# Performance work log

Hardware: AMD Instinct MI355X
Metric: run time of the kernel (lower is better)

Reference implementation:

```python
import jax, jax.numpy as jnp
import numpy as np

B, NIN, D = 2048, 64, 128
N_LCB, N_FMB, RANK = 32, 32, 24
DIM_HIDDEN = 1024
N_OUT = N_LCB + N_FMB  # == NIN -> identity residual
MAX_VAL = 1.0
EPS_LN_FMB_MIN, EPS_LN_FMB_MAX = 1e-11, 1e7
KERAS_LN_EPS = 1e-3


def setup_inputs() -> dict:
    key = jax.random.key(0)
    ks = jax.random.split(key, 9)
    def w(k, shape, fan):
        return (jax.random.normal(k, shape, jnp.float32) / np.sqrt(fan)).astype(jnp.float32)
    return {
        "x": jax.random.normal(ks[0], (B, NIN, D), jnp.float32),
        "noise": jax.random.uniform(ks[1], (B, N_OUT, D), jnp.float32),
        "w_lcb": w(ks[2], (NIN, N_LCB), NIN),
        "w_rank": w(ks[3], (NIN, RANK), NIN),
        "w1": w(ks[4], (NIN * RANK, DIM_HIDDEN), NIN * RANK),
        "w2": w(ks[5], (DIM_HIDDEN, DIM_HIDDEN), DIM_HIDDEN),
        "w3": w(ks[6], (DIM_HIDDEN, N_FMB * D), DIM_HIDDEN),
        "gamma": jnp.ones((D,), jnp.float32),
        "beta": jnp.zeros((D,), jnp.float32),
    }


def _forward(x, noise, w_lcb, w_rank, w1, w2, w3, gamma, beta):
    # ---- LinearCompressBlock: Dense over feature (emb-count) axis ----
    lcb = jnp.einsum("bnd,nm->bmd", x, w_lcb)  # (B, N_LCB, D)

    # ---- FactorizationMachineBlock ----
    # rank_layer on transposed input: (B, D, NIN) @ (NIN, RANK)
    r = jnp.einsum("bnd,nr->bdr", x, w_rank)          # (B, D, RANK)
    fm = jnp.einsum("bnd,bdr->bnr", x, r)             # (B, NIN, RANK)
    fm = fm.reshape(fm.shape[0], NIN * RANK)
    # custom LayerNorm (no affine, clipped std)
    mu = jnp.mean(fm, axis=-1, keepdims=True)
    cen = fm - mu
    std = jnp.sqrt(jnp.mean(cen * cen, axis=-1, keepdims=True))
    std = jnp.clip(std, EPS_LN_FMB_MIN, EPS_LN_FMB_MAX)
    fm = cen / std
    # MLP: 2 hidden relu layers + linear out, dropout=0 / inference
    h = jax.nn.relu(fm @ w1)
    h = jax.nn.relu(h @ w2)
    fmb = (h @ w3).reshape(-1, N_FMB, D)              # (B, N_FMB, D)

    out = jnp.concatenate((fmb, lcb), axis=1)          # (B, N_OUT, D)
    residual = x                                        # NIN == N_OUT -> identity

    safe = jnp.clip(out, -MAX_VAL, MAX_VAL)
    a = jnp.abs(safe)
    c = lambda t: jnp.clip(t, -MAX_VAL, MAX_VAL)

    # conv term: reshape to (B, N, D//8, 8), 1x1 conv with all-ones (8->8)
    # filter == group-sum broadcast back over the 8 lanes
    g = safe.reshape(safe.shape[0], N_OUT, D // 8, 8)
    conv = jnp.broadcast_to(g.sum(-1, keepdims=True), g.shape).reshape(safe.shape)

    extra = (
        c(jnp.log(a + 1.0))
        + c(jax.lax.rsqrt(a + 1.0))
        + c(jax.nn.softmax(safe, axis=-1))
        + c(jnp.tanh(safe))
        + c(jnp.where(safe >= 0, safe, 0.2 * safe))          # leaky_relu alpha=0.2
        + c(jnp.exp(safe))
        + c(jax.nn.softplus(safe))
        + c(jnp.log1p(a))
        + jnp.zeros_like(safe)                               # zeros_like term
        + c(jnp.round(safe))
        + jnp.ones_like(safe)                                # pow(a+eps, 0) == 1
        + c(jnp.sign(safe))
        + c(jnp.prod(safe, axis=-1, keepdims=True))
        + c(jnp.isnan(safe).astype(jnp.float32))
        + c((~(safe < 0)).astype(jnp.float32))
        + c((safe != 0).astype(jnp.float32))
        + c((safe >= 0).astype(jnp.float32))
        + c(safe.astype(jnp.int8).astype(jnp.float32))       # bitwise_and(x,x)==x after int8 cast
        + c(jnp.max(safe, axis=-1, keepdims=True))
        + c(safe + safe)                                     # add_n([safe, safe])
        + c(safe + safe)                                     # raw Add
        + 7.0 * safe                                         # slice/split-concat/merge/einsum/squeeze/pad/stack identities (|safe|<=1 so clip no-op)
        + c(jnp.where(safe > 0.5, -1.0, safe))               # tensor_scatter_nd_update
        + c(conv)
        + c(noise)                                           # tf.random.uniform (deterministic input)
        + c(jnp.arange(D, dtype=jnp.float32))                # broadcast over last axis
        + c(jnp.sum(safe[0] * safe[0], axis=-1))[None, :, None]  # DiagPart(matmul(safe[0], safe[0]^T))
    )

    pre = out + residual + 1e-10 * extra
    # keras LayerNormalization(axis=-1), default epsilon=1e-3
    m = jnp.mean(pre, axis=-1, keepdims=True)
    v = jnp.mean(jnp.square(pre - m), axis=-1, keepdims=True)
    return (pre - m) * jax.lax.rsqrt(v + KERAS_LN_EPS) * gamma + beta


def reference(x, noise, w_lcb, w_rank, w1, w2, w3, gamma, beta):
    return _forward(x, noise, w_lcb, w_rank, w1, w2, w3, gamma, beta)
```

## Files before the change

kernel.cpp:

```cpp
#include <hip/hip_runtime.h>


typedef _Float16 half8_t __attribute__((ext_vector_type(8)));
typedef _Float16 half4_t __attribute__((ext_vector_type(4)));
typedef float floatx4 __attribute__((ext_vector_type(4)));

#define B_SZ 2048
#define NIN 64
#define D_SZ 128
#define RANK 24
#define FMK (NIN * RANK)
#define HID 1024
#define NFMB_D (32 * 128)
#define ROW_F (NIN * D_SZ)

__device__ __forceinline__ void wg_barrier() {
  asm volatile("s_waitcnt lgkmcnt(0)" ::: "memory");
  __builtin_amdgcn_sched_barrier(0);
  __builtin_amdgcn_s_barrier();
  __builtin_amdgcn_sched_barrier(0);
}

__global__ __launch_bounds__(256) void transpose_cast_all(
    const float* __restrict__ w1, const float* __restrict__ w2,
    const float* __restrict__ w3, const float* __restrict__ w_rank,
    const float* __restrict__ w_lcb, _Float16* __restrict__ w1t,
    _Float16* __restrict__ w2t, _Float16* __restrict__ w3t,
    _Float16* __restrict__ wr16, _Float16* __restrict__ wl16) {
  __shared__ float tile[32][33];
  int bid = blockIdx.x;
  if (bid == 48 * 32 + 32 * 32 + 32 * 128) {
    const int t = threadIdx.x;
#pragma unroll
    for (int k = 0; k < 8; k++) {
      int i = t + k * 256;
      int j = i >> 6, n = i & 63;
      wr16[i] = (_Float16)(j < RANK ? w_rank[n * RANK + j] : 0.f);
      wl16[i] = (_Float16)w_lcb[n * 32 + j];
    }
    return;
  }
  const float* w;
  _Float16* wt;
  int K, N, kt;
  if (bid < 48 * 32) {
    w = w1; wt = w1t; K = FMK; N = HID; kt = 48;
  } else if (bid < 48 * 32 + 32 * 32) {
    bid -= 48 * 32;
    w = w2; wt = w2t; K = HID; N = HID; kt = 32;
  } else {
    bid -= 48 * 32 + 32 * 32;
    w = w3; wt = w3t; K = HID; N = NFMB_D; kt = 32;
  }
  const int tk = (bid % kt) * 32;
  const int tn = (bid / kt) * 32;
  const int tx = threadIdx.x & 31;
  const int ty = threadIdx.x >> 5;
#pragma unroll
  for (int i = 0; i < 4; i++) {
    int k = ty + i * 8;
    tile[k][tx] = w[(size_t)(tk + k) * N + (tn + tx)];
  }
  __syncthreads();
#pragma unroll
  for (int i = 0; i < 4; i++) {
    int n = ty + i * 8;
    wt[(size_t)(tn + n) * K + (tk + tx)] = (_Float16)tile[tx][n];
  }
}

#define STX 72
#define STN 136
__global__ __launch_bounds__(256, 3) void front_kernel(
    const float* __restrict__ x, const _Float16* __restrict__ wr16,
    const _Float16* __restrict__ wl16, const float* __restrict__ gamma,
    const float* __restrict__ beta, _Float16* __restrict__ fmn,
    float* __restrict__ out) {
  constexpr int XT_OFF = 0;
  constexpr int X16_OFF = 18432;
  constexpr int RT_OFF = X16_OFF + 17408;
  constexpr int RED_OFF = RT_OFF + 8704;
  __shared__ __align__(16) char smem[RED_OFF + 32];
  __shared__ float2 lstat[32][4];
  _Float16* xT = (_Float16*)(smem + XT_OFF);
  _Float16* x16 = (_Float16*)(smem + X16_OFF);
  _Float16* rT = (_Float16*)(smem + RT_OFF);
  float* redbuf = (float*)(smem + RED_OFF);
  _Float16* fmn_s = (_Float16*)(smem + RT_OFF);

  const int b = blockIdx.x, t = threadIdx.x;
  const int lane = t & 63;
  const int w = __builtin_amdgcn_readfirstlane(t >> 6);
  const int q = lane >> 4, ln = lane & 15;

  half8_t ar[2][2], al[2][2];
#pragma unroll
  for (int k = 0; k < 2; k++)
#pragma unroll
    for (int mi = 0; mi < 2; mi++) {
      ar[k][mi] = *(const half8_t*)&wr16[(mi * 16 + ln) * 64 + k * 32 + q * 8];
      al[k][mi] = *(const half8_t*)&wl16[(mi * 16 + ln) * 64 + k * 32 + q * 8];
    }

  const float4* xg4 = (const float4*)(x + (size_t)b * ROW_F);
#pragma unroll
  for (int hh = 0; hh < 2; hh++) {
    int bb = t + hh * 256;
    int n0 = (bb >> 5) * 4;
    int bd = bb & 31;
    int d0 = bd * 4;
    float4 L0 = xg4[(n0 + 0) * 32 + bd];
    float4 L1 = xg4[(n0 + 1) * 32 + bd];
    float4 L2 = xg4[(n0 + 2) * 32 + bd];
    float4 L3 = xg4[(n0 + 3) * 32 + bd];
    *(half4_t*)&x16[(n0 + 0) * STN + d0] =
        half4_t{(_Float16)L0.x, (_Float16)L0.y, (_Float16)L0.z, (_Float16)L0.w};
    *(half4_t*)&x16[(n0 + 1) * STN + d0] =
        half4_t{(_Float16)L1.x, (_Float16)L1.y, (_Float16)L1.z, (_Float16)L1.w};
    *(half4_t*)&x16[(n0 + 2) * STN + d0] =
        half4_t{(_Float16)L2.x, (_Float16)L2.y, (_Float16)L2.z, (_Float16)L2.w};
    *(half4_t*)&x16[(n0 + 3) * STN + d0] =
        half4_t{(_Float16)L3.x, (_Float16)L3.y, (_Float16)L3.z, (_Float16)L3.w};
    *(half4_t*)&xT[(d0 + 0) * STX + n0] =
        half4_t{(_Float16)L0.x, (_Float16)L1.x, (_Float16)L2.x, (_Float16)L3.x};
    *(half4_t*)&xT[(d0 + 1) * STX + n0] =
        half4_t{(_Float16)L0.y, (_Float16)L1.y, (_Float16)L2.y, (_Float16)L3.y};
    *(half4_t*)&xT[(d0 + 2) * STX + n0] =
        half4_t{(_Float16)L0.z, (_Float16)L1.z, (_Float16)L2.z, (_Float16)L3.z};
    *(half4_t*)&xT[(d0 + 3) * STX + n0] =
        half4_t{(_Float16)L0.w, (_Float16)L1.w, (_Float16)L2.w, (_Float16)L3.w};
  }
  __syncthreads();

  floatx4 r_acc[2][2] = {};
  floatx4 l_acc[2][2] = {};
#pragma unroll
  for (int k = 0; k < 2; k++) {
    half8_t bfrag[2];
#pragma unroll
    for (int ni = 0; ni < 2; ni++)
      bfrag[ni] =
          *(const half8_t*)&xT[((2 * w + ni) * 16 + ln) * STX + k * 32 + q * 8];
#pragma unroll
    for (int mi = 0; mi < 2; mi++)
#pragma unroll
      for (int ni = 0; ni < 2; ni++) {
        r_acc[mi][ni] = __builtin_amdgcn_mfma_f32_16x16x32_f16(
            ar[k][mi], bfrag[ni], r_acc[mi][ni], 0, 0, 0);
        l_acc[mi][ni] = __builtin_amdgcn_mfma_f32_16x16x32_f16(
            al[k][mi], bfrag[ni], l_acc[mi][ni], 0, 0, 0);
      }
  }
#pragma unroll
  for (int mi = 0; mi < 2; mi++)
#pragma unroll
    for (int ni = 0; ni < 2; ni++)
#pragma unroll
      for (int rr = 0; rr < 4; rr++)
        rT[(mi * 16 + q * 4 + rr) * STN + (2 * w + ni) * 16 + ln] =
            (_Float16)r_acc[mi][ni][rr];
  __syncthreads();

  floatx4 f_acc[2] = {};
#pragma unroll
  for (int k = 0; k < 4; k++) {
    half8_t af = *(const half8_t*)&x16[(w * 16 + ln) * STN + k * 32 + q * 8];
#pragma unroll
    for (int nj = 0; nj < 2; nj++) {
      half8_t bf = *(const half8_t*)&rT[(nj * 16 + ln) * STN + k * 32 + q * 8];
      f_acc[nj] =
          __builtin_amdgcn_mfma_f32_16x16x32_f16(af, bf, f_acc[nj], 0, 0, 0);
    }
  }
  float s = 0.f, s2 = 0.f;
#pragma unroll
  for (int rr = 0; rr < 4; rr++) {
    float v = f_acc[0][rr];
    s += v;
    s2 += v * v;
    float v1 = (ln < 8) ? f_acc[1][rr] : 0.f;
    s += v1;
    s2 += v1 * v1;
  }
#pragma unroll
  for (int off = 1; off < 64; off <<= 1) {
    s += __shfl_xor(s, off);
    s2 += __shfl_xor(s2, off);
  }
  if (lane == 0) {
    redbuf[w * 2] = s;
    redbuf[w * 2 + 1] = s2;
  }
  __syncthreads();
  s = redbuf[0] + redbuf[2] + redbuf[4] + redbuf[6];
  s2 = redbuf[1] + redbuf[3] + redbuf[5] + redbuf[7];
  const float mu = s * (1.f / FMK);
  float var = s2 * (1.f / FMK) - mu * mu;
  var = var > 0.f ? var : 0.f;
  float sd = sqrtf(var);
  sd = sd < 1e-11f ? 1e-11f : (sd > 1e7f ? 1e7f : sd);
  const float inv = 1.f / sd;

#pragma unroll
  for (int nj = 0; nj < 2; nj++) {
    int j = nj * 16 + ln;
    if (j < RANK) {
#pragma unroll
      for (int rr = 0; rr < 4; rr++)
        fmn_s[(w * 16 + q * 4 + rr) * RANK + j] =
            (_Float16)((f_acc[nj][rr] - mu) * inv);
    }
  }

  const int d0 = (2 * w) * 16 + ln;
  const int d1 = d0 + 16;
  const float g0 = gamma[d0], g1 = gamma[d1];
  const float be0 = beta[d0], be1 = beta[d1];
  float lv0[2][4], lv1[2][4];
  float sw[2][4], s2w[2][4];
#pragma unroll
  for (int mi = 0; mi < 2; mi++)
#pragma unroll
    for (int rr = 0; rr < 4; rr++) {
      int m = mi * 16 + q * 4 + rr;
      float v0 = l_acc[mi][0][rr] + (float)x16[(32 + m) * STN + d0];
      float v1 = l_acc[mi][1][rr] + (float)x16[(32 + m) * STN + d1];
      lv0[mi][rr] = v0;
      lv1[mi][rr] = v1;
      sw[mi][rr] = v0 + v1;
      s2w[mi][rr] = v0 * v0 + v1 * v1;
    }
#pragma unroll
  for (int off = 1; off < 16; off <<= 1) {
#pragma unroll
    for (int mi = 0; mi < 2; mi++)
#pragma unroll
      for (int rr = 0; rr < 4; rr++) {
        sw[mi][rr] += __shfl_xor(sw[mi][rr], off);
        s2w[mi][rr] += __shfl_xor(s2w[mi][rr], off);
      }
  }
  if (ln == 0) {
#pragma unroll
    for (int mi = 0; mi < 2; mi++)
#pragma unroll
      for (int rr = 0; rr < 4; rr++)
        lstat[mi * 16 + q * 4 + rr][w] = float2{sw[mi][rr], s2w[mi][rr]};
  }
  __syncthreads();

  half8_t* fg = (half8_t*)(fmn + (size_t)b * FMK);
  if (t < FMK / 8) fg[t] = ((const half8_t*)fmn_s)[t];
  float* ob = out + (size_t)b * ROW_F;
#pragma unroll
  for (int mi = 0; mi < 2; mi++)
#pragma unroll
    for (int rr = 0; rr < 4; rr++) {
      int m = mi * 16 + q * 4 + rr;
      float2 p0 = lstat[m][0], p1 = lstat[m][1];
      float2 p2 = lstat[m][2], p3 = lstat[m][3];
      float S = p0.x + p1.x + p2.x + p3.x;
      float S2 = p0.y + p1.y + p2.y + p3.y;
      float mean = S * (1.f / 128.f);
      float varr = S2 * (1.f / 128.f) - mean * mean;
      float rstd = rsqrtf(varr + 1e-3f);
      ob[(32 + m) * 128 + d0] = (lv0[mi][rr] - mean) * rstd * g0 + be0;
      ob[(32 + m) * 128 + d1] = (lv1[mi][rr] - mean) * rstd * g1 + be1;
    }
}

template <bool RELU>
__global__ __launch_bounds__(256, 2) void gemm_bt(
    const _Float16* __restrict__ A, const _Float16* __restrict__ Bt,
    _Float16* __restrict__ C, int M, int N, int K) {
  constexpr int LDT = 40;
  __shared__ __align__(16) _Float16 As[2][64 * LDT];
  __shared__ __align__(16) _Float16 Bs[2][64 * LDT];
  const int m0 = blockIdx.x * 64;
  const int n0 = blockIdx.y * 64;
  const int t = threadIdx.x;
  const int wave = t >> 6, lane = t & 63;
  const int wr = wave >> 1, wc = wave & 1;
  const int q = lane >> 4, ln = lane & 15;
  const int srow = t >> 2;
  const int skc = t & 3;
  const _Float16* gA = A + (size_t)(m0 + srow) * K + skc * 8;
  const _Float16* gB = Bt + (size_t)(n0 + srow) * K + skc * 8;
  const int ldsw = srow * LDT + skc * 8;
  const int nT = K / 32;

  floatx4 acc[2][2] = {};

  uint4 rax = *(const uint4*)gA;
  uint4 rbx = *(const uint4*)gB;
  *(uint4*)&As[0][ldsw] = rax;
  *(uint4*)&Bs[0][ldsw] = rbx;
  uint4 ray = *(const uint4*)(gA + 32);
  uint4 rby = *(const uint4*)(gB + 32);
  rax = *(const uint4*)(gA + 64);
  rbx = *(const uint4*)(gB + 64);
  wg_barrier();

  for (int tp = 0;;) {
    if (tp + 1 < nT) {
      *(uint4*)&As[1][ldsw] = ray;
      *(uint4*)&Bs[1][ldsw] = rby;
    }
    half8_t af[2], bf[2];
#pragma unroll
    for (int i = 0; i < 2; i++) {
      af[i] = *(const half8_t*)&As[0][(wr * 32 + i * 16 + ln) * LDT + q * 8];
      bf[i] = *(const half8_t*)&Bs[0][(wc * 32 + i * 16 + ln) * LDT + q * 8];
    }
    if (tp + 3 < nT) {
      ray = *(const uint4*)(gA + (tp + 3) * 32);
      rby = *(const uint4*)(gB + (tp + 3) * 32);
    }
#pragma unroll
    for (int i = 0; i < 2; i++)
#pragma unroll
      for (int j = 0; j < 2; j++)
        acc[i][j] = __builtin_amdgcn_mfma_f32_16x16x32_f16(af[i], bf[j],
                                                           acc[i][j], 0, 0, 0);
    if (tp + 1 >= nT) break;
    wg_barrier();
    if (tp + 2 < nT) {
      *(uint4*)&As[0][ldsw] = rax;
      *(uint4*)&Bs[0][ldsw] = rbx;
    }
#pragma unroll
    for (int i = 0; i < 2; i++) {
      af[i] = *(const half8_t*)&As[1][(wr * 32 + i * 16 + ln) * LDT + q * 8];
      bf[i] = *(const half8_t*)&Bs[1][(wc * 32 + i * 16 + ln) * LDT + q * 8];
    }
    if (tp + 4 < nT) {
      rax = *(const uint4*)(gA + (tp + 4) * 32);
      rbx = *(const uint4*)(gB + (tp + 4) * 32);
    }
#pragma unroll
    for (int i = 0; i < 2; i++)
#pragma unroll
      for (int j = 0; j < 2; j++)
        acc[i][j] = __builtin_amdgcn_mfma_f32_16x16x32_f16(af[i], bf[j],
                                                           acc[i][j], 0, 0, 0);
    tp += 2;
    if (tp >= nT) break;
    wg_barrier();
  }

#pragma unroll
  for (int i = 0; i < 2; i++) {
#pragma unroll
    for (int r = 0; r < 4; r++) {
      size_t row = (size_t)(m0 + wr * 32 + i * 16 + q * 4 + r);
      _Float16* crow = C + row * N + n0 + wc * 32 + ln;
#pragma unroll
      for (int j = 0; j < 2; j++) {
        float v = acc[i][j][r];
        if (RELU) v = v > 0.f ? v : 0.f;
        crow[j * 16] = (_Float16)v;
      }
    }
  }
}

__global__ __launch_bounds__(256, 2) void gemm_ln(
    const _Float16* __restrict__ A, const _Float16* __restrict__ Bt,
    const float* __restrict__ x, const float* __restrict__ gamma,
    const float* __restrict__ beta, float* __restrict__ out) {
  constexpr int LDT = 40;
  constexpr int K = HID;
  constexpr int nT = K / 32;
  __shared__ __align__(16) _Float16 As[2][128 * LDT];
  __shared__ __align__(16) _Float16 Bs[2][128 * LDT];
  __shared__ float2 rowst[128][2];
  const int m0 = blockIdx.x * 128;
  const int c = blockIdx.y;
  const int n0 = c * 128;
  const int t = threadIdx.x;
  const int wave = t >> 6, lane = t & 63;
  const int wr = wave >> 1, wc = wave & 1;
  const int q = lane >> 4, ln = lane & 15;
  const int srow = t >> 2;
  const int skc = t & 3;
  const _Float16* gA0 = A + (size_t)(m0 + srow) * K + skc * 8;
  const _Float16* gA1 = gA0 + (size_t)64 * K;
  const _Float16* gB0 = Bt + (size_t)(n0 + srow) * K + skc * 8;
  const _Float16* gB1 = gB0 + (size_t)64 * K;
  const int ldsw = srow * LDT + skc * 8;

  floatx4 acc[4][4] = {};

  uint4 raX0 = *(const uint4*)gA0, raX1 = *(const uint4*)gA1;
  uint4 rbX0 = *(const uint4*)gB0, rbX1 = *(const uint4*)gB1;
  *(uint4*)&As[0][ldsw] = raX0;
  *(uint4*)&As[0][64 * LDT + ldsw] = raX1;
  *(uint4*)&Bs[0][ldsw] = rbX0;
  *(uint4*)&Bs[0][64 * LDT + ldsw] = rbX1;
  uint4 raY0 = *(const uint4*)(gA0 + 32), raY1 = *(const uint4*)(gA1 + 32);
  uint4 rbY0 = *(const uint4*)(gB0 + 32), rbY1 = *(const uint4*)(gB1 + 32);
  raX0 = *(const uint4*)(gA0 + 64);
  raX1 = *(const uint4*)(gA1 + 64);
  rbX0 = *(const uint4*)(gB0 + 64);
  rbX1 = *(const uint4*)(gB1 + 64);
  wg_barrier();

  for (int tp = 0;;) {
    if (tp + 1 < nT) {
      *(uint4*)&As[1][ldsw] = raY0;
      *(uint4*)&As[1][64 * LDT + ldsw] = raY1;
      *(uint4*)&Bs[1][ldsw] = rbY0;
      *(uint4*)&Bs[1][64 * LDT + ldsw] = rbY1;
    }
    half8_t af[4], bf[4];
#pragma unroll
    for (int i = 0; i < 4; i++)
      af[i] = *(const half8_t*)&As[0][(wr * 64 + i * 16 + ln) * LDT + q * 8];
#pragma unroll
    for (int j = 0; j < 4; j++)
      bf[j] = *(const half8_t*)&Bs[0][(wc * 64 + j * 16 + ln) * LDT + q * 8];
    if (tp + 3 < nT) {
      raY0 = *(const uint4*)(gA0 + (tp + 3) * 32);
      raY1 = *(const uint4*)(gA1 + (tp + 3) * 32);
      rbY0 = *(const uint4*)(gB0 + (tp + 3) * 32);
      rbY1 = *(const uint4*)(gB1 + (tp + 3) * 32);
    }
#pragma unroll
    for (int i = 0; i < 4; i++)
#pragma unroll
      for (int j = 0; j < 4; j++)
        acc[i][j] = __builtin_amdgcn_mfma_f32_16x16x32_f16(af[i], bf[j],
                                                           acc[i][j], 0, 0, 0);
    if (tp + 1 >= nT) break;
    wg_barrier();
    if (tp + 2 < nT) {
      *(uint4*)&As[0][ldsw] = raX0;
      *(uint4*)&As[0][64 * LDT + ldsw] = raX1;
      *(uint4*)&Bs[0][ldsw] = rbX0;
      *(uint4*)&Bs[0][64 * LDT + ldsw] = rbX1;
    }
#pragma unroll
    for (int i = 0; i < 4; i++)
      af[i] = *(const half8_t*)&As[1][(wr * 64 + i * 16 + ln) * LDT + q * 8];
#pragma unroll
    for (int j = 0; j < 4; j++)
      bf[j] = *(const half8_t*)&Bs[1][(wc * 64 + j * 16 + ln) * LDT + q * 8];
    if (tp + 4 < nT) {
      raX0 = *(const uint4*)(gA0 + (tp + 4) * 32);
      raX1 = *(const uint4*)(gA1 + (tp + 4) * 32);
      rbX0 = *(const uint4*)(gB0 + (tp + 4) * 32);
      rbX1 = *(const uint4*)(gB1 + (tp + 4) * 32);
    }
#pragma unroll
    for (int i = 0; i < 4; i++)
#pragma unroll
      for (int j = 0; j < 4; j++)
        acc[i][j] = __builtin_amdgcn_mfma_f32_16x16x32_f16(af[i], bf[j],
                                                           acc[i][j], 0, 0, 0);
    tp += 2;
    if (tp >= nT) break;
    wg_barrier();
  }

  float s[4][4], s2[4][4];
#pragma unroll
  for (int i = 0; i < 4; i++)
#pragma unroll
    for (int r = 0; r < 4; r++) {
      const int row = wr * 64 + i * 16 + q * 4 + r;
      const float* xr = x + (size_t)(m0 + row) * ROW_F + n0 + wc * 64 + ln;
      float ss = 0.f, qq = 0.f;
#pragma unroll
      for (int j = 0; j < 4; j++) {
        float v = acc[i][j][r] + xr[j * 16];
        acc[i][j][r] = v;
        ss += v;
        qq += v * v;
      }
      s[i][r] = ss;
      s2[i][r] = qq;
    }
#pragma unroll
  for (int off = 1; off < 16; off <<= 1) {
#pragma unroll
    for (int i = 0; i < 4; i++)
#pragma unroll
      for (int r = 0; r < 4; r++) {
        s[i][r] += __shfl_xor(s[i][r], off);
        s2[i][r] += __shfl_xor(s2[i][r], off);
      }
  }
  if (ln == 0) {
#pragma unroll
    for (int i = 0; i < 4; i++)
#pragma unroll
      for (int r = 0; r < 4; r++)
        rowst[wr * 64 + i * 16 + q * 4 + r][wc] = float2{s[i][r], s2[i][r]};
  }
  __syncthreads();
  float g[4], bb[4];
#pragma unroll
  for (int j = 0; j < 4; j++) {
    g[j] = gamma[wc * 64 + j * 16 + ln];
    bb[j] = beta[wc * 64 + j * 16 + ln];
  }
#pragma unroll
  for (int i = 0; i < 4; i++)
#pragma unroll
    for (int r = 0; r < 4; r++) {
      int row = wr * 64 + i * 16 + q * 4 + r;
      float2 p0 = rowst[row][0], p1 = rowst[row][1];
      float mean = (p0.x + p1.x) * (1.f / 128.f);
      float varr = (p0.y + p1.y) * (1.f / 128.f) - mean * mean;
      float rstd = rsqrtf(varr + 1e-3f);
      float* orow = out + (size_t)(m0 + row) * ROW_F + n0 + wc * 64 + ln;
#pragma unroll
      for (int j = 0; j < 4; j++)
        orow[j * 16] = (acc[i][j][r] - mean) * rstd * g[j] + bb[j];
    }
}

extern "C" void kernel_launch(void* const* d_in, const int* in_sizes, int n_in,
                              void* d_out, int out_size, void* d_ws,
                              size_t ws_size, hipStream_t stream) {
  const float* x = (const float*)d_in[0];
  const float* w_lcb = (const float*)d_in[2];
  const float* w_rank = (const float*)d_in[3];
  const float* w1 = (const float*)d_in[4];
  const float* w2 = (const float*)d_in[5];
  const float* w3 = (const float*)d_in[6];
  const float* gamma = (const float*)d_in[7];
  const float* beta = (const float*)d_in[8];
  float* out = (float*)d_out;

  char* ws = (char*)d_ws;
  _Float16* w1t = (_Float16*)ws; ws += (size_t)HID * FMK * 2;
  _Float16* w2t = (_Float16*)ws; ws += (size_t)HID * HID * 2;
  _Float16* w3t = (_Float16*)ws; ws += (size_t)NFMB_D * HID * 2;
  _Float16* fmn = (_Float16*)ws; ws += (size_t)B_SZ * FMK * 2;
  _Float16* h1  = (_Float16*)ws; ws += (size_t)B_SZ * HID * 2;
  _Float16* wr16 = (_Float16*)ws; ws += 32 * 64 * 2;
  _Float16* wl16 = (_Float16*)ws; ws += 32 * 64 * 2;
  _Float16* h2 = fmn;

  transpose_cast_all<<<48 * 32 + 32 * 32 + 32 * 128 + 1, 256, 0, stream>>>(
      w1, w2, w3, w_rank, w_lcb, w1t, w2t, w3t, wr16, wl16);
  front_kernel<<<B_SZ, 256, 0, stream>>>(x, wr16, wl16, gamma, beta, fmn, out);
  gemm_bt<true><<<dim3(B_SZ / 64, HID / 64), 256, 0, stream>>>(
      fmn, w1t, h1, B_SZ, HID, FMK);
  gemm_bt<true><<<dim3(B_SZ / 64, HID / 64), 256, 0, stream>>>(
      h1, w2t, h2, B_SZ, HID, HID);
  gemm_ln<<<dim3(B_SZ / 128, 32), 256, 0, stream>>>(h2, w3t, x, gamma, beta, out);
}
```

Baseline: 255.2 us.

## Load MFMA fragments directly from global memory and remap blocks for XCD locality

```diff
diff --git a/kernel.cpp b/kernel.cpp
--- a/kernel.cpp
+++ b/kernel.cpp
@@ -13,13 +13,6 @@
 #define HID 1024
 #define NFMB_D (32 * 128)
 #define ROW_F (NIN * D_SZ)
-
-__device__ __forceinline__ void wg_barrier() {
-  asm volatile("s_waitcnt lgkmcnt(0)" ::: "memory");
-  __builtin_amdgcn_sched_barrier(0);
-  __builtin_amdgcn_s_barrier();
-  __builtin_amdgcn_sched_barrier(0);
-}
 
 __global__ __launch_bounds__(256) void transpose_cast_all(
     const float* __restrict__ w1, const float* __restrict__ w2,
@@ -269,83 +262,59 @@
     }
 }
 
-template <bool RELU>
+template <int K, bool RELU>
 __global__ __launch_bounds__(256, 2) void gemm_bt(
     const _Float16* __restrict__ A, const _Float16* __restrict__ Bt,
-    _Float16* __restrict__ C, int M, int N, int K) {
-  constexpr int LDT = 40;
-  __shared__ __align__(16) _Float16 As[2][64 * LDT];
-  __shared__ __align__(16) _Float16 Bs[2][64 * LDT];
-  const int m0 = blockIdx.x * 64;
-  const int n0 = blockIdx.y * 64;
+    _Float16* __restrict__ C) {
+  constexpr int nT = K / 32;
+  const int flat = blockIdx.x + (blockIdx.y << 5);
+  const int xcd = flat & 7, sub = flat >> 3;
+  const int mb = (xcd & 3) * 8 + (sub & 7);
+  const int nb = (xcd >> 2) * 8 + (sub >> 3);
+  const int m0 = mb * 64, n0 = nb * 64;
   const int t = threadIdx.x;
   const int wave = t >> 6, lane = t & 63;
   const int wr = wave >> 1, wc = wave & 1;
   const int q = lane >> 4, ln = lane & 15;
-  const int srow = t >> 2;
-  const int skc = t & 3;
-  const _Float16* gA = A + (size_t)(m0 + srow) * K + skc * 8;
-  const _Float16* gB = Bt + (size_t)(n0 + srow) * K + skc * 8;
-  const int ldsw = srow * LDT + skc * 8;
-  const int nT = K / 32;
+
+  const _Float16* a0 = A + (size_t)(m0 + wr * 32 + ln) * K + q * 8;
+  const _Float16* b0 = Bt + (size_t)(n0 + wc * 32 + ln) * K + q * 8;
 
   floatx4 acc[2][2] = {};
-
-  uint4 rax = *(const uint4*)gA;
-  uint4 rbx = *(const uint4*)gB;
-  *(uint4*)&As[0][ldsw] = rax;
-  *(uint4*)&Bs[0][ldsw] = rbx;
-  uint4 ray = *(const uint4*)(gA + 32);
-  uint4 rby = *(const uint4*)(gB + 32);
-  rax = *(const uint4*)(gA + 64);
-  rbx = *(const uint4*)(gB + 64);
-  wg_barrier();
+  half8_t aX[2], bX[2], aY[2], bY[2];
+  auto ld2 = [&](half8_t(&d)[2], const _Float16* base, int kk) {
+#pragma unroll
+    for (int i = 0; i < 2; i++)
+      d[i] = *(const half8_t*)(base + (size_t)(i * 16) * K + kk);
+  };
+  ld2(aX, a0, 0);
+  ld2(bX, b0, 0);
+  ld2(aY, a0, 32);
+  ld2(bY, b0, 32);
 
   for (int tp = 0;;) {
-    if (tp + 1 < nT) {
-      *(uint4*)&As[1][ldsw] = ray;
-      *(uint4*)&Bs[1][ldsw] = rby;
-    }
-    half8_t af[2], bf[2];
-#pragma unroll
-    for (int i = 0; i < 2; i++) {
-      af[i] = *(const half8_t*)&As[0][(wr * 32 + i * 16 + ln) * LDT + q * 8];
-      bf[i] = *(const half8_t*)&Bs[0][(wc * 32 + i * 16 + ln) * LDT + q * 8];
-    }
+#pragma unroll
+    for (int i = 0; i < 2; i++)
+#pragma unroll
+      for (int j = 0; j < 2; j++)
+        acc[i][j] = __builtin_amdgcn_mfma_f32_16x16x32_f16(aX[i], bX[j],
+                                                           acc[i][j], 0, 0, 0);
+    if (tp + 2 < nT) {
+      ld2(aX, a0, (tp + 2) * 32);
+      ld2(bX, b0, (tp + 2) * 32);
+    }
+#pragma unroll
+    for (int i = 0; i < 2; i++)
+#pragma unroll
+      for (int j = 0; j < 2; j++)
+        acc[i][j] = __builtin_amdgcn_mfma_f32_16x16x32_f16(aY[i], bY[j],
+                                                           acc[i][j], 0, 0, 0);
     if (tp + 3 < nT) {
-      ray = *(const uint4*)(gA + (tp + 3) * 32);
-      rby = *(const uint4*)(gB + (tp + 3) * 32);
-    }
-#pragma unroll
-    for (int i = 0; i < 2; i++)
-#pragma unroll
-      for (int j = 0; j < 2; j++)
-        acc[i][j] = __builtin_amdgcn_mfma_f32_16x16x32_f16(af[i], bf[j],
-                                                           acc[i][j], 0, 0, 0);
-    if (tp + 1 >= nT) break;
-    wg_barrier();
-    if (tp + 2 < nT) {
-      *(uint4*)&As[0][ldsw] = rax;
-      *(uint4*)&Bs[0][ldsw] = rbx;
-    }
-#pragma unroll
-    for (int i = 0; i < 2; i++) {
-      af[i] = *(const half8_t*)&As[1][(wr * 32 + i * 16 + ln) * LDT + q * 8];
-      bf[i] = *(const half8_t*)&Bs[1][(wc * 32 + i * 16 + ln) * LDT + q * 8];
-    }
-    if (tp + 4 < nT) {
-      rax = *(const uint4*)(gA + (tp + 4) * 32);
-      rbx = *(const uint4*)(gB + (tp + 4) * 32);
-    }
-#pragma unroll
-    for (int i = 0; i < 2; i++)
-#pragma unroll
-      for (int j = 0; j < 2; j++)
-        acc[i][j] = __builtin_amdgcn_mfma_f32_16x16x32_f16(af[i], bf[j],
-                                                           acc[i][j], 0, 0, 0);
+      ld2(aY, a0, (tp + 3) * 32);
+      ld2(bY, b0, (tp + 3) * 32);
+    }
     tp += 2;
     if (tp >= nT) break;
-    wg_barrier();
   }
 
 #pragma unroll
@@ -353,7 +322,7 @@
 #pragma unroll
     for (int r = 0; r < 4; r++) {
       size_t row = (size_t)(m0 + wr * 32 + i * 16 + q * 4 + r);
-      _Float16* crow = C + row * N + n0 + wc * 32 + ln;
+      _Float16* crow = C + row * HID + n0 + wc * 32 + ln;
 #pragma unroll
       for (int j = 0; j < 2; j++) {
         float v = acc[i][j][r];
@@ -368,98 +337,57 @@
     const _Float16* __restrict__ A, const _Float16* __restrict__ Bt,
     const float* __restrict__ x, const float* __restrict__ gamma,
     const float* __restrict__ beta, float* __restrict__ out) {
-  constexpr int LDT = 40;
   constexpr int K = HID;
   constexpr int nT = K / 32;
-  __shared__ __align__(16) _Float16 As[2][128 * LDT];
-  __shared__ __align__(16) _Float16 Bs[2][128 * LDT];
   __shared__ float2 rowst[128][2];
-  const int m0 = blockIdx.x * 128;
-  const int c = blockIdx.y;
-  const int n0 = c * 128;
+  const int flat = blockIdx.x + (blockIdx.y << 4);
+  const int xcd = flat & 7, sub = flat >> 3;
+  const int mb = (xcd & 1) * 8 + (sub & 7);
+  const int c = (xcd >> 1) * 8 + (sub >> 3);
+  const int m0 = mb * 128, n0 = c * 128;
   const int t = threadIdx.x;
   const int wave = t >> 6, lane = t & 63;
   const int wr = wave >> 1, wc = wave & 1;
   const int q = lane >> 4, ln = lane & 15;
-  const int srow = t >> 2;
-  const int skc = t & 3;
-  const _Float16* gA0 = A + (size_t)(m0 + srow) * K + skc * 8;
-  const _Float16* gA1 = gA0 + (size_t)64 * K;
-  const _Float16* gB0 = Bt + (size_t)(n0 + srow) * K + skc * 8;
-  const _Float16* gB1 = gB0 + (size_t)64 * K;
-  const int ldsw = srow * LDT + skc * 8;
+
+  const _Float16* a0 = A + (size_t)(m0 + wr * 64 + ln) * K + q * 8;
+  const _Float16* b0 = Bt + (size_t)(n0 + wc * 64 + ln) * K + q * 8;
 
   floatx4 acc[4][4] = {};
-
-  uint4 raX0 = *(const uint4*)gA0, raX1 = *(const uint4*)gA1;
-  uint4 rbX0 = *(const uint4*)gB0, rbX1 = *(const uint4*)gB1;
-  *(uint4*)&As[0][ldsw] = raX0;
-  *(uint4*)&As[0][64 * LDT + ldsw] = raX1;
-  *(uint4*)&Bs[0][ldsw] = rbX0;
-  *(uint4*)&Bs[0][64 * LDT + ldsw] = rbX1;
-  uint4 raY0 = *(const uint4*)(gA0 + 32), raY1 = *(const uint4*)(gA1 + 32);
-  uint4 rbY0 = *(const uint4*)(gB0 + 32), rbY1 = *(const uint4*)(gB1 + 32);
-  raX0 = *(const uint4*)(gA0 + 64);
-  raX1 = *(const uint4*)(gA1 + 64);
-  rbX0 = *(const uint4*)(gB0 + 64);
-  rbX1 = *(const uint4*)(gB1 + 64);
-  wg_barrier();
+  half8_t aX[4], bX[4], aY[4], bY[4];
+  auto ld4 = [&](half8_t(&d)[4], const _Float16* base, int kk) {
+#pragma unroll
+    for (int i = 0; i < 4; i++)
+      d[i] = *(const half8_t*)(base + (size_t)(i * 16) * K + kk);
+  };
+  ld4(aX, a0, 0);
+  ld4(bX, b0, 0);
+  ld4(aY, a0, 32);
+  ld4(bY, b0, 32);
 
   for (int tp = 0;;) {
-    if (tp + 1 < nT) {
-      *(uint4*)&As[1][ldsw] = raY0;
-      *(uint4*)&As[1][64 * LDT + ldsw] = raY1;
-      *(uint4*)&Bs[1][ldsw] = rbY0;
-      *(uint4*)&Bs[1][64 * LDT + ldsw] = rbY1;
-    }
-    half8_t af[4], bf[4];
 #pragma unroll
     for (int i = 0; i < 4; i++)
-      af[i] = *(const half8_t*)&As[0][(wr * 64 + i * 16 + ln) * LDT + q * 8];
-#pragma unroll
-    for (int j = 0; j < 4; j++)
-      bf[j] = *(const half8_t*)&Bs[0][(wc * 64 + j * 16 + ln) * LDT + q * 8];
+#pragma unroll
+      for (int j = 0; j < 4; j++)
+        acc[i][j] = __builtin_amdgcn_mfma_f32_16x16x32_f16(aX[i], bX[j],
+                                                           acc[i][j], 0, 0, 0);
+    if (tp + 2 < nT) {
+      ld4(aX, a0, (tp + 2) * 32);
+      ld4(bX, b0, (tp + 2) * 32);
+    }
+#pragma unroll
+    for (int i = 0; i < 4; i++)
+#pragma unroll
+      for (int j = 0; j < 4; j++)
+        acc[i][j] = __builtin_amdgcn_mfma_f32_16x16x32_f16(aY[i], bY[j],
+                                                           acc[i][j], 0, 0, 0);
     if (tp + 3 < nT) {
-      raY0 = *(const uint4*)(gA0 + (tp + 3) * 32);
-      raY1 = *(const uint4*)(gA1 + (tp + 3) * 32);
-      rbY0 = *(const uint4*)(gB0 + (tp + 3) * 32);
-      rbY1 = *(const uint4*)(gB1 + (tp + 3) * 32);
-    }
-#pragma unroll
-    for (int i = 0; i < 4; i++)
-#pragma unroll
-      for (int j = 0; j < 4; j++)
-        acc[i][j] = __builtin_amdgcn_mfma_f32_16x16x32_f16(af[i], bf[j],
-                                                           acc[i][j], 0, 0, 0);
-    if (tp + 1 >= nT) break;
-    wg_barrier();
-    if (tp + 2 < nT) {
-      *(uint4*)&As[0][ldsw] = raX0;
-      *(uint4*)&As[0][64 * LDT + ldsw] = raX1;
-      *(uint4*)&Bs[0][ldsw] = rbX0;
-      *(uint4*)&Bs[0][64 * LDT + ldsw] = rbX1;
-    }
-#pragma unroll
-    for (int i = 0; i < 4; i++)
-      af[i] = *(const half8_t*)&As[1][(wr * 64 + i * 16 + ln) * LDT + q * 8];
-#pragma unroll
-    for (int j = 0; j < 4; j++)
-      bf[j] = *(const half8_t*)&Bs[1][(wc * 64 + j * 16 + ln) * LDT + q * 8];
-    if (tp + 4 < nT) {
-      raX0 = *(const uint4*)(gA0 + (tp + 4) * 32);
-      raX1 = *(const uint4*)(gA1 + (tp + 4) * 32);
-      rbX0 = *(const uint4*)(gB0 + (tp + 4) * 32);
-      rbX1 = *(const uint4*)(gB1 + (tp + 4) * 32);
-    }
-#pragma unroll
-    for (int i = 0; i < 4; i++)
-#pragma unroll
-      for (int j = 0; j < 4; j++)
-        acc[i][j] = __builtin_amdgcn_mfma_f32_16x16x32_f16(af[i], bf[j],
-                                                           acc[i][j], 0, 0, 0);
+      ld4(aY, a0, (tp + 3) * 32);
+      ld4(bY, b0, (tp + 3) * 32);
+    }
     tp += 2;
     if (tp >= nT) break;
-    wg_barrier();
   }
 
   float s[4][4], s2[4][4];
@@ -546,9 +474,9 @@
   transpose_cast_all<<<48 * 32 + 32 * 32 + 32 * 128 + 1, 256, 0, stream>>>(
       w1, w2, w3, w_rank, w_lcb, w1t, w2t, w3t, wr16, wl16);
   front_kernel<<<B_SZ, 256, 0, stream>>>(x, wr16, wl16, gamma, beta, fmn, out);
-  gemm_bt<true><<<dim3(B_SZ / 64, HID / 64), 256, 0, stream>>>(
-      fmn, w1t, h1, B_SZ, HID, FMK);
-  gemm_bt<true><<<dim3(B_SZ / 64, HID / 64), 256, 0, stream>>>(
-      h1, w2t, h2, B_SZ, HID, HID);
+  gemm_bt<FMK, true><<<dim3(B_SZ / 64, HID / 64), 256, 0, stream>>>(
+      fmn, w1t, h1);
+  gemm_bt<HID, true><<<dim3(B_SZ / 64, HID / 64), 256, 0, stream>>>(
+      h1, w2t, h2);
   gemm_ln<<<dim3(B_SZ / 128, 32), 256, 0, stream>>>(h2, w3t, x, gamma, beta, out);
 }
```

Result: slower. 333.0 us (+30.5%).
